# Optimization experiments

Hardware: AMD Instinct MI355X
Metric: run time of the kernel (lower is better)

The kernel has to match this reference:

```python
import jax, jax.numpy as jnp
import numpy as np

B, D, DK = 16384, 1024, 1024


def setup_inputs() -> dict:
    key = jax.random.key(0)
    ks = jax.random.split(key, 11)
    return {
        "x": jax.random.normal(ks[0], (B, D), jnp.float32),
        "x_prev": jax.random.normal(ks[1], (B, D), jnp.float32),
        "num": jax.random.uniform(ks[2], (B, DK), jnp.float32),
        "den": jax.random.uniform(ks[3], (B, DK), jnp.float32) + 1.0,
        "Wk": jax.random.normal(ks[4], (DK, D), jnp.float32) * (D ** -0.5),
        "bk": jnp.zeros((DK,), jnp.float32),
        "mix_k": jax.random.uniform(ks[5], (), jnp.float32),
        "Wf": jax.random.normal(ks[6], (D, DK), jnp.float32) * (DK ** -0.5),
        "bf": jnp.zeros((D,), jnp.float32),
        "bonus": jax.random.normal(ks[7], (DK,), jnp.float32) * 0.1,
        "decay": jnp.float32(0.2),
    }


def reference(x, x_prev, num, den, Wk, bk, mix_k, Wf, bf, bonus, decay):
    # MixingLinear: Linear(mix*x + (1-mix)*x_prev). Source uses Kmaker for
    # K, R and V, so all three equal this single projection (faithful to code).
    mixed = mix_k * x + (1.0 - mix_k) * x_prev          # [B, D]
    K = mixed @ Wk.T + bk                                # [B, DK]; K == R == V
    e_bk = jnp.exp(bonus + K)                            # [B, DK]
    wkv = (num + e_bk * K) / (den + e_bk)                # V = K
    rwkv = jax.nn.sigmoid(K) * wkv                       # R = K
    w = jnp.exp(-jnp.exp(decay))                         # scalar time-decay
    eK = jnp.exp(K)
    num_new = w * num + eK * K                           # V = K
    den_new = w * den + eK
    out = rwkv @ Wf.T + bf                               # [B, D]
    return out, num_new, den_new
```

## Files before the change

### kernel.cpp

```cpp
#include <hip/hip_runtime.h>
#include <cstdint>

#define DEV static __device__ __forceinline__

typedef float f32x4 __attribute__((ext_vector_type(4)));
typedef short bf16x8 __attribute__((ext_vector_type(8)));

constexpr int Bsz = 16384;
constexpr int Dd  = 1024;
constexpr int DKd = 1024;

DEV unsigned short f2bf(float f) {
    uint32_t u = __builtin_bit_cast(uint32_t, f);
    u += 0x7FFFu + ((u >> 16) & 1u);
    return (unsigned short)(u >> 16);
}

DEV void async_lds16(const void* g, void* l) {
    __builtin_amdgcn_global_load_lds(
        (const __attribute__((address_space(1))) void*)g,
        (__attribute__((address_space(3))) void*)l,
        16, 0, 0);
}

__global__ void k_prep(const float4* __restrict__ x, const float4* __restrict__ xp,
                       const float* __restrict__ mixp,
                       const float4* __restrict__ Wk, const float4* __restrict__ Wf,
                       unsigned short* __restrict__ mixed,
                       unsigned short* __restrict__ WkB,
                       unsigned short* __restrict__ WfB) {
    constexpr int n_mix = Bsz * Dd / 4;
    constexpr int n_w   = DKd * Dd / 4;
    constexpr int total = n_mix + 2 * n_w;
    const float m = *mixp, m1 = 1.0f - m;
    int i = blockIdx.x * blockDim.x + threadIdx.x;
    const int st = gridDim.x * blockDim.x;
    for (; i < total; i += st) {
        float4 a;
        unsigned short* dst;
        int idx;
        if (i < n_mix) {
            float4 xa = x[i], xb = xp[i];
            a.x = m * xa.x + m1 * xb.x;
            a.y = m * xa.y + m1 * xb.y;
            a.z = m * xa.z + m1 * xb.z;
            a.w = m * xa.w + m1 * xb.w;
            dst = mixed; idx = i;
        } else if (i < n_mix + n_w) {
            a = Wk[i - n_mix]; dst = WkB; idx = i - n_mix;
        } else {
            a = Wf[i - n_mix - n_w]; dst = WfB; idx = i - n_mix - n_w;
        }
        ushort4 o;
        o.x = f2bf(a.x); o.y = f2bf(a.y); o.z = f2bf(a.z); o.w = f2bf(a.w);
        reinterpret_cast<ushort4*>(dst)[idx] = o;
    }
}

template <int EPI>
__global__ __launch_bounds__(512)
void k_gemm(const unsigned short* __restrict__ A,
            const unsigned short* __restrict__ Bw,
            const float* __restrict__ bias,
            const float* __restrict__ num, const float* __restrict__ den,
            const float* __restrict__ bonus, const float* __restrict__ decayp,
            float* __restrict__ o0,
            float* __restrict__ o1,
            unsigned short* __restrict__ orw)
{
    __shared__ __align__(16) unsigned short As[2][256 * 64];
    __shared__ __align__(16) unsigned short Bs[2][256 * 64];

    const int tid = threadIdx.x;
    const int bid = (int)blockIdx.x;
    const int xcd = bid & 7;
    const int cb  = xcd >> 1;
    const int rb  = ((xcd & 1) << 5) + (bid >> 3);
    const int row0 = rb * 256;
    const int col0 = cb * 256;

    const int lane = tid & 63;
    const int wid  = tid >> 6;
    const int wr = wid >> 2, wc = wid & 3;
    const int l16 = lane & 15, lq = lane >> 4;
    const int xm = l16 & 7;

    const int r0 = tid >> 3;
    const int cg = (tid & 7) ^ (r0 & 7);
    const unsigned short* pa[4];
    const unsigned short* pb[4];
#pragma unroll
    for (int i = 0; i < 4; ++i) {
        pa[i] = A  + (size_t)(row0 + i * 64 + r0) * 1024 + cg * 8;
        pb[i] = Bw + (size_t)(col0 + i * 64 + r0) * 1024 + cg * 8;
    }
    unsigned short* la = &As[0][tid * 8];
    unsigned short* lb = &Bs[0][tid * 8];

    const int jj0 = (lq ^ xm) * 8;
    const int jj1 = ((4 + lq) ^ xm) * 8;
    const int aoff0 = (wr * 128 + l16) * 64 + jj0;
    const int aoff1 = (wr * 128 + l16) * 64 + jj1;
    const int boff0 = (wc * 64 + l16) * 64 + jj0;
    const int boff1 = (wc * 64 + l16) * 64 + jj1;

    f32x4 acc[8][4] = {};

    auto stage = [&](int buf, int kt) {
        const int ko = kt * 64;
        const int lo = buf * (256 * 64);
#pragma unroll
        for (int i = 0; i < 4; ++i)
            async_lds16(pa[i] + ko, la + lo + i * 4096);
#pragma unroll
        for (int i = 0; i < 4; ++i)
            async_lds16(pb[i] + ko, lb + lo + i * 4096);
    };

    stage(0, 0);
    __syncthreads();

#pragma unroll
    for (int kt = 0; kt < 16; ++kt) {
        const int cur = kt & 1;
        if (kt < 15) stage(cur ^ 1, kt + 1);
        const unsigned short* Ab = &As[0][cur * (256 * 64)];
        const unsigned short* Bb = &Bs[0][cur * (256 * 64)];
#pragma unroll
        for (int kk = 0; kk < 2; ++kk) {
            const int ao = kk ? aoff1 : aoff0;
            const int bo = kk ? boff1 : boff0;
            bf16x8 af[8], bfr[4];
#pragma unroll
            for (int n = 0; n < 4; ++n)
                bfr[n] = *reinterpret_cast<const bf16x8*>(Bb + bo + n * 1024);
#pragma unroll
            for (int m = 0; m < 8; ++m)
                af[m] = *reinterpret_cast<const bf16x8*>(Ab + ao + m * 1024);
#pragma unroll
            for (int m = 0; m < 8; ++m)
#pragma unroll
                for (int n = 0; n < 4; ++n)
                    acc[m][n] = __builtin_amdgcn_mfma_f32_16x16x32_bf16(
                        af[m], bfr[n], acc[m][n], 0, 0, 0);
        }
        __syncthreads();
    }

    const int baserow = row0 + wr * 128 + lq * 4;
    const int basecol = col0 + wc * 64 + l16;

    if constexpr (EPI == 1) {
        const float w_decay = __expf(-__expf(*decayp));
        float cbias[4], cebon[4];
#pragma unroll
        for (int n = 0; n < 4; ++n) {
            cbias[n] = bias[basecol + n * 16];
            cebon[n] = __expf(bonus[basecol + n * 16]);
        }
#pragma unroll
        for (int m = 0; m < 8; ++m) {
#pragma unroll
            for (int r = 0; r < 4; ++r) {
                const size_t rowoff = (size_t)(baserow + m * 16 + r) * 1024;
#pragma unroll
                for (int n = 0; n < 4; ++n) {
                    const size_t idx = rowoff + basecol + n * 16;
                    const float Kv  = acc[m][n][r] + cbias[n];
                    const float eK  = __expf(Kv);
                    const float ebk = cebon[n] * eK;
                    const float nb  = num[idx];
                    const float db  = den[idx];
                    const float wkv = (nb + ebk * Kv) * __builtin_amdgcn_rcpf(db + ebk);
                    const float sig = eK * __builtin_amdgcn_rcpf(1.0f + eK);
                    o0[idx]  = w_decay * nb + eK * Kv;
                    o1[idx]  = w_decay * db + eK;
                    orw[idx] = f2bf(sig * wkv);
                }
            }
        }
    } else {
        float cbias[4];
#pragma unroll
        for (int n = 0; n < 4; ++n) cbias[n] = bias[basecol + n * 16];
#pragma unroll
        for (int m = 0; m < 8; ++m) {
#pragma unroll
            for (int r = 0; r < 4; ++r) {
                const size_t rowoff = (size_t)(baserow + m * 16 + r) * 1024;
#pragma unroll
                for (int n = 0; n < 4; ++n)
                    o0[rowoff + basecol + n * 16] = acc[m][n][r] + cbias[n];
            }
        }
    }
}

extern "C" void kernel_launch(void* const* d_in, const int* in_sizes, int n_in,
                              void* d_out, int out_size, void* d_ws, size_t ws_size,
                              hipStream_t stream) {
    const float* x     = (const float*)d_in[0];
    const float* xprev = (const float*)d_in[1];
    const float* num   = (const float*)d_in[2];
    const float* den   = (const float*)d_in[3];
    const float* Wk    = (const float*)d_in[4];
    const float* bk    = (const float*)d_in[5];
    const float* mixk  = (const float*)d_in[6];
    const float* Wf    = (const float*)d_in[7];
    const float* bf_   = (const float*)d_in[8];
    const float* bonus = (const float*)d_in[9];
    const float* decay = (const float*)d_in[10];

    float* out    = (float*)d_out;
    float* numnew = out + (size_t)Bsz * Dd;
    float* dennew = numnew + (size_t)Bsz * DKd;

    char* ws = (char*)d_ws;
    unsigned short* mixed = (unsigned short*)ws;
    unsigned short* WkB   = (unsigned short*)(ws + (size_t)Bsz * Dd * 2);
    unsigned short* WfB   = WkB + (size_t)DKd * Dd;
    unsigned short* rwkv  = WfB + (size_t)Dd * DKd;

    k_prep<<<2048, 256, 0, stream>>>((const float4*)x, (const float4*)xprev, mixk,
                                     (const float4*)Wk, (const float4*)Wf,
                                     mixed, WkB, WfB);

    const int grid = (Bsz / 256) * (DKd / 256);
    k_gemm<1><<<grid, 512, 0, stream>>>(mixed, WkB, bk, num, den, bonus, decay,
                                        numnew, dennew, rwkv);
    k_gemm<0><<<grid, 512, 0, stream>>>(rwkv, WfB, bf_, nullptr, nullptr, nullptr,
                                        nullptr, out, nullptr, nullptr);
}
```

Before: 205.8 us.

## Shrink GEMM tiles to 128x128 with single-buffered LDS and 256 threads

Shrinks the GEMM block tile from 256x256 (512 threads) to 128x128 (256 threads). LDS drops from double-buffered to single-buffered with a load-sync-compute-sync loop, and the XCD-aware block mapping becomes a plain row/column split. The smaller per-block footprint and accumulator count should allow more blocks per CU, letting occupancy hide latency instead of explicit prefetch. The trade-off is lower data reuse per tile, more global and L2 traffic, and no overlap of loads with MFMA inside a block.

```diff
diff --git a/kernel.cpp b/kernel.cpp
--- a/kernel.cpp
+++ b/kernel.cpp
@@ -58,7 +58,7 @@
 }
 
 template <int EPI>
-__global__ __launch_bounds__(512)
+__global__ __launch_bounds__(256)
 void k_gemm(const unsigned short* __restrict__ A,
             const unsigned short* __restrict__ Bw,
             const float* __restrict__ bias,
@@ -68,20 +68,19 @@
             float* __restrict__ o1,
             unsigned short* __restrict__ orw)
 {
-    __shared__ __align__(16) unsigned short As[2][256 * 64];
-    __shared__ __align__(16) unsigned short Bs[2][256 * 64];
+    __shared__ __align__(16) unsigned short As[128 * 64];
+    __shared__ __align__(16) unsigned short Bs[128 * 64];
 
     const int tid = threadIdx.x;
     const int bid = (int)blockIdx.x;
-    const int xcd = bid & 7;
-    const int cb  = xcd >> 1;
-    const int rb  = ((xcd & 1) << 5) + (bid >> 3);
-    const int row0 = rb * 256;
-    const int col0 = cb * 256;
+    const int cb  = bid & 7;
+    const int rb  = bid >> 3;
+    const int row0 = rb * 128;
+    const int col0 = cb * 128;
 
     const int lane = tid & 63;
     const int wid  = tid >> 6;
-    const int wr = wid >> 2, wc = wid & 3;
+    const int wr = wid >> 1, wc = wid & 1;
     const int l16 = lane & 15, lq = lane >> 4;
     const int xm = l16 & 7;
 
@@ -91,54 +90,45 @@
     const unsigned short* pb[4];
 #pragma unroll
     for (int i = 0; i < 4; ++i) {
-        pa[i] = A  + (size_t)(row0 + i * 64 + r0) * 1024 + cg * 8;
-        pb[i] = Bw + (size_t)(col0 + i * 64 + r0) * 1024 + cg * 8;
-    }
-    unsigned short* la = &As[0][tid * 8];
-    unsigned short* lb = &Bs[0][tid * 8];
+        pa[i] = A  + (size_t)(row0 + i * 32 + r0) * 1024 + cg * 8;
+        pb[i] = Bw + (size_t)(col0 + i * 32 + r0) * 1024 + cg * 8;
+    }
+    unsigned short* la = &As[tid * 8];
+    unsigned short* lb = &Bs[tid * 8];
 
     const int jj0 = (lq ^ xm) * 8;
     const int jj1 = ((4 + lq) ^ xm) * 8;
-    const int aoff0 = (wr * 128 + l16) * 64 + jj0;
-    const int aoff1 = (wr * 128 + l16) * 64 + jj1;
+    const int aoff0 = (wr * 64 + l16) * 64 + jj0;
+    const int aoff1 = (wr * 64 + l16) * 64 + jj1;
     const int boff0 = (wc * 64 + l16) * 64 + jj0;
     const int boff1 = (wc * 64 + l16) * 64 + jj1;
 
-    f32x4 acc[8][4] = {};
-
-    auto stage = [&](int buf, int kt) {
+    f32x4 acc[4][4] = {};
+
+#pragma unroll 1
+    for (int kt = 0; kt < 16; ++kt) {
         const int ko = kt * 64;
-        const int lo = buf * (256 * 64);
 #pragma unroll
         for (int i = 0; i < 4; ++i)
-            async_lds16(pa[i] + ko, la + lo + i * 4096);
+            async_lds16(pa[i] + ko, la + i * 2048);
 #pragma unroll
         for (int i = 0; i < 4; ++i)
-            async_lds16(pb[i] + ko, lb + lo + i * 4096);
-    };
-
-    stage(0, 0);
-    __syncthreads();
-
-#pragma unroll
-    for (int kt = 0; kt < 16; ++kt) {
-        const int cur = kt & 1;
-        if (kt < 15) stage(cur ^ 1, kt + 1);
-        const unsigned short* Ab = &As[0][cur * (256 * 64)];
-        const unsigned short* Bb = &Bs[0][cur * (256 * 64)];
+            async_lds16(pb[i] + ko, lb + i * 2048);
+        __syncthreads();
+
 #pragma unroll
         for (int kk = 0; kk < 2; ++kk) {
             const int ao = kk ? aoff1 : aoff0;
             const int bo = kk ? boff1 : boff0;
-            bf16x8 af[8], bfr[4];
+            bf16x8 af[4], bfr[4];
 #pragma unroll
             for (int n = 0; n < 4; ++n)
-                bfr[n] = *reinterpret_cast<const bf16x8*>(Bb + bo + n * 1024);
-#pragma unroll
-            for (int m = 0; m < 8; ++m)
-                af[m] = *reinterpret_cast<const bf16x8*>(Ab + ao + m * 1024);
-#pragma unroll
-            for (int m = 0; m < 8; ++m)
+                bfr[n] = *reinterpret_cast<const bf16x8*>(&Bs[bo + n * 1024]);
+#pragma unroll
+            for (int m = 0; m < 4; ++m)
+                af[m] = *reinterpret_cast<const bf16x8*>(&As[ao + m * 1024]);
+#pragma unroll
+            for (int m = 0; m < 4; ++m)
 #pragma unroll
                 for (int n = 0; n < 4; ++n)
                     acc[m][n] = __builtin_amdgcn_mfma_f32_16x16x32_bf16(
@@ -147,7 +137,7 @@
         __syncthreads();
     }
 
-    const int baserow = row0 + wr * 128 + lq * 4;
+    const int baserow = row0 + wr * 64 + lq * 4;
     const int basecol = col0 + wc * 64 + l16;
 
     if constexpr (EPI == 1) {
@@ -159,7 +149,7 @@
             cebon[n] = __expf(bonus[basecol + n * 16]);
         }
 #pragma unroll
-        for (int m = 0; m < 8; ++m) {
+        for (int m = 0; m < 4; ++m) {
 #pragma unroll
             for (int r = 0; r < 4; ++r) {
                 const size_t rowoff = (size_t)(baserow + m * 16 + r) * 1024;
@@ -184,7 +174,7 @@
 #pragma unroll
         for (int n = 0; n < 4; ++n) cbias[n] = bias[basecol + n * 16];
 #pragma unroll
-        for (int m = 0; m < 8; ++m) {
+        for (int m = 0; m < 4; ++m) {
 #pragma unroll
             for (int r = 0; r < 4; ++r) {
                 const size_t rowoff = (size_t)(baserow + m * 16 + r) * 1024;
@@ -225,9 +215,9 @@
                                      (const float4*)Wk, (const float4*)Wf,
                                      mixed, WkB, WfB);
 
-    const int grid = (Bsz / 256) * (DKd / 256);
-    k_gemm<1><<<grid, 512, 0, stream>>>(mixed, WkB, bk, num, den, bonus, decay,
+    const int grid = (Bsz / 128) * (DKd / 128);
+    k_gemm<1><<<grid, 256, 0, stream>>>(mixed, WkB, bk, num, den, bonus, decay,
                                         numnew, dennew, rwkv);
-    k_gemm<0><<<grid, 512, 0, stream>>>(rwkv, WfB, bf_, nullptr, nullptr, nullptr,
+    k_gemm<0><<<grid, 256, 0, stream>>>(rwkv, WfB, bf_, nullptr, nullptr, nullptr,
                                         nullptr, out, nullptr, nullptr);
 }
```

Result: slower. 210.7 us (+2.4%).
